# Kernel optimization log

Measured on AMD Instinct MI355X. Metric: run time of the kernel, lower is better.

The kernel has to match this reference:

```python
import jax, jax.numpy as jnp
import numpy as np

RES = 512
MAX_DEPTH = 100.0
AMBIENT = 0.3
LIGHT_STREN = 0.8
SHININESS = 16.0
EPS = 1e-8


def _unit(v):
    return v / (jnp.linalg.norm(v, axis=-1, keepdims=True) + EPS)


def setup_inputs() -> dict:
    key = jax.random.key(0)
    ks = jax.random.split(key, 8)
    B, N, M, TEX = 1, 512, 128, 512
    verts = jax.random.uniform(ks[0], (B, N, 3), minval=-1.0, maxval=1.0, dtype=jnp.float32)
    faces = jax.random.randint(ks[1], (B, M, 3), 0, N, dtype=jnp.int32)
    normals = jax.random.normal(ks[2], (B, M, 3, 3), dtype=jnp.float32)
    uvs = jax.random.uniform(ks[3], (B, M, 3, 2), dtype=jnp.float32)
    textures = jax.random.uniform(ks[4], (B, TEX, TEX, 3), dtype=jnp.float32)
    f = RES / 2.0
    K = jnp.array([[f, 0.0, RES / 2.0], [0.0, f, RES / 2.0], [0.0, 0.0, 1.0]], jnp.float32)
    Ks = jnp.broadcast_to(K, (B, 3, 3))
    RT = jnp.concatenate([jnp.eye(3, dtype=jnp.float32), jnp.array([[0.0], [0.0], [2.0]], jnp.float32)], axis=1)
    RTs = jnp.broadcast_to(RT, (B, 3, 4))
    view_dir = jax.random.normal(ks[5], (B, 3), dtype=jnp.float32)
    light_dir = jax.random.normal(ks[6], (B, 3), dtype=jnp.float32)
    return {"verts": verts, "faces": faces, "normals": normals, "uvs": uvs,
            "textures": textures, "Ks": Ks, "RTs": RTs, "view_dir": view_dir, "light_dir": light_dir}


def _render(verts, faces, normals, uvs, textures, Ks, RTs, view_dir, light_dir):
    B = verts.shape[0]
    # camera space: cam = R @ v + t
    cam = jnp.einsum('bij,bnj->bni', RTs[:, :, :3], verts) + RTs[:, None, :, 3]
    # orthographic projection to pixel coords
    x = Ks[:, None, 0, 0] * cam[..., 0] + Ks[:, None, 0, 2]
    y = Ks[:, None, 1, 1] * cam[..., 1] + Ks[:, None, 1, 2]
    xy = jnp.stack([x, y], -1)            # [B,N,2]
    z = cam[..., 2]                        # [B,N]
    gather_v = jax.vmap(lambda a, f: a[f])
    tv = gather_v(xy, faces)               # [B,M,3,2] screen-space triangle corners
    tz = gather_v(z, faces)                # [B,M,3]
    # pixel centers, row-major (p = row*RES + col)
    ii = jnp.arange(RES, dtype=jnp.float32) + 0.5
    py, px = jnp.meshgrid(ii, ii, indexing='ij')
    pix = jnp.stack([px.ravel(), py.ravel()], -1)   # [P,2]

    def edge(a, b, p):
        return (b[..., 0] - a[..., 0]) * (p[..., 1] - a[..., 1]) - (b[..., 1] - a[..., 1]) * (p[..., 0] - a[..., 0])

    v0, v1, v2 = tv[:, None, :, 0], tv[:, None, :, 1], tv[:, None, :, 2]  # [B,1,M,2]
    p = pix[None, :, None]                                               # [1,P,1,2]
    w0 = edge(v1, v2, p)                   # [B,P,M]
    w1 = edge(v2, v0, p)
    w2 = edge(v0, v1, p)
    area = w0 + w1 + w2
    inside = (((w0 >= 0) & (w1 >= 0) & (w2 >= 0)) | ((w0 <= 0) & (w1 <= 0) & (w2 <= 0))) & (jnp.abs(area) > EPS)
    inv_a = 1.0 / jnp.where(jnp.abs(area) > EPS, area, 1.0)
    zpix = (w0 * tz[:, None, :, 0] + w1 * tz[:, None, :, 1] + w2 * tz[:, None, :, 2]) * inv_a
    valid = inside & (zpix > 0)
    zc = jnp.where(valid, zpix, MAX_DEPTH)   # [B,P,M] candidate depths
    depth = jnp.min(zc, axis=-1)             # z-buffer result [B,P]
    win = jnp.argmin(zc, axis=-1)             # winning triangle per pixel [B,P]
    hit = depth < MAX_DEPTH

    # recompute barycentrics for the winning triangle only (avoids [B,P,M,3])
    gpick = jax.vmap(lambda a, i: a[i])
    tvw = gpick(tv, win)                      # [B,P,3,2]
    nw = gpick(normals, win)                  # [B,P,3,3]
    uvw = gpick(uvs, win)                     # [B,P,3,2]
    pp = pix[None]                            # [1,P,2]

    def e2(a, b):
        return (b[..., 0] - a[..., 0]) * (pp[..., 1] - a[..., 1]) - (b[..., 1] - a[..., 1]) * (pp[..., 0] - a[..., 0])

    u0 = e2(tvw[:, :, 1], tvw[:, :, 2])
    u1 = e2(tvw[:, :, 2], tvw[:, :, 0])
    u2 = e2(tvw[:, :, 0], tvw[:, :, 1])
    ar = u0 + u1 + u2
    inv2 = 1.0 / jnp.where(jnp.abs(ar) > EPS, ar, 1.0)
    bary = jnp.stack([u0, u1, u2], -1) * inv2[..., None]   # [B,P,3]
    nrm = _unit(jnp.einsum('bpk,bpkc->bpc', bary, nw))     # interpolated normal
    uv = jnp.einsum('bpk,bpkc->bpc', bary, uvw)            # interpolated uv [B,P,2]

    # bilinear texture sampling
    Ht, Wt = textures.shape[1], textures.shape[2]
    uu = jnp.clip(uv[..., 0], 0.0, 1.0) * (Wt - 1)
    vv = jnp.clip(uv[..., 1], 0.0, 1.0) * (Ht - 1)
    x0 = jnp.floor(uu).astype(jnp.int32)
    y0 = jnp.floor(vv).astype(jnp.int32)
    x1 = jnp.minimum(x0 + 1, Wt - 1)
    y1 = jnp.minimum(y0 + 1, Ht - 1)
    fx = (uu - x0.astype(jnp.float32))[..., None]
    fy = (vv - y0.astype(jnp.float32))[..., None]
    tget = jax.vmap(lambda t, a, b: t[a, b])
    col = (tget(textures, y0, x0) * (1 - fx) * (1 - fy) + tget(textures, y0, x1) * fx * (1 - fy)
           + tget(textures, y1, x0) * (1 - fx) * fy + tget(textures, y1, x1) * fx * fy)  # [B,P,3]

    # Lambert diffuse + Blinn-Phong specular
    ld = _unit(light_dir)
    vd = _unit(view_dir)
    diff = jnp.clip(jnp.einsum('bpc,bc->bp', nrm, ld), 0.0)
    h = _unit(ld + vd)
    spec = LIGHT_STREN * jnp.clip(jnp.einsum('bpc,bc->bp', nrm, h), 0.0) ** SHININESS
    shade = col * (AMBIENT + LIGHT_STREN * diff)[..., None] + spec[..., None]
    rgb = jnp.where(hit[..., None], shade, 0.0)

    depths = depth.reshape(B, RES, RES)
    rgbs = rgb.reshape(B, RES, RES, 3)
    masks = hit.reshape(B, RES, RES).astype(jnp.int32)
    return depths, rgbs, masks


def reference(verts, faces, normals, uvs, textures, Ks, RTs, view_dir, light_dir):
    return _render(verts, faces, normals, uvs, textures, Ks, RTs, view_dir, light_dir)
```

## Files before the change

kernel.cpp:

```cpp
#include <hip/hip_runtime.h>
#include <math.h>

#pragma clang fp contract(off)

#define RES         512
#define TILE        16
#define TILESX      (RES / TILE)
#define MAXF        128
#define MAX_DEPTH   100.0f
#define AMBIENT     0.3f
#define LIGHT_STREN 0.8f
#define EPSF        1e-8f
#define MARG        1.0f
#define ZGUARD      1e-3f

struct __attribute__((packed, aligned(4))) PF4 { float a, b, c, d; };
struct __attribute__((packed, aligned(4))) PF2 { float a, b; };
static __device__ __forceinline__ PF4 ld4(const float* p) { PF4 v; __builtin_memcpy(&v, p, 16); return v; }
static __device__ __forceinline__ PF2 ld2(const float* p) { PF2 v; __builtin_memcpy(&v, p, 8); return v; }

__global__ __launch_bounds__(256) void mesh_render_tiled(
    const float* __restrict__ verts,
    const int*   __restrict__ faces,
    const float* __restrict__ normals,
    const float* __restrict__ uvs,
    const float* __restrict__ tex,
    const float* __restrict__ Ks,
    const float* __restrict__ RTs,
    const float* __restrict__ view_dir,
    const float* __restrict__ light_dir,
    float* __restrict__ out,
    int M, int TEXW, int TEXH)
{
    __shared__ float4 smA[MAXF];
    __shared__ float4 smB[MAXF];
    __shared__ float2 smC[MAXF];
    __shared__ int    cid[MAXF];
    __shared__ int    scnt[2][8];
    __shared__ float  slit[6];

    const int tid = threadIdx.x;
    const int tx  = blockIdx.x % TILESX;
    const int ty  = blockIdx.x / TILESX;
    const float PX0 = (float)(tx * TILE) + 0.5f;
    const float PY0 = (float)(ty * TILE) + 0.5f;

    bool flag = false;
    int  bkt  = -1;
    float X0=0,Y0=0,Z0=0, X1=0,Y1=0,Z1=0, X2=0,Y2=0,Z2=0, MZ=0;
    unsigned long long bmask = 0;

    if (tid < MAXF) {
        if (tid < M) {
            const float r00 = RTs[0], r01 = RTs[1], r02 = RTs[2],  t0 = RTs[3];
            const float r10 = RTs[4], r11 = RTs[5], r12 = RTs[6],  t1 = RTs[7];
            const float r20 = RTs[8], r21 = RTs[9], r22 = RTs[10], t2 = RTs[11];
            const float k00 = Ks[0], k02 = Ks[2], k11 = Ks[4], k12 = Ks[5];
            float X[3], Y[3], Z[3];
            #pragma unroll
            for (int k = 0; k < 3; ++k) {
                int vi = faces[tid * 3 + k];
                float vx = verts[vi * 3 + 0];
                float vy = verts[vi * 3 + 1];
                float vz = verts[vi * 3 + 2];
                float cx = ((r00 * vx + r01 * vy) + r02 * vz) + t0;
                float cy = ((r10 * vx + r11 * vy) + r12 * vz) + t1;
                float cz = ((r20 * vx + r21 * vy) + r22 * vz) + t2;
                X[k] = k00 * cx + k02;
                Y[k] = k11 * cy + k12;
                Z[k] = cz;
            }
            X0=X[0]; Y0=Y[0]; Z0=Z[0]; X1=X[1]; Y1=Y[1]; Z1=Z[1];
            X2=X[2]; Y2=Y[2]; Z2=Z[2];
            MZ = fminf(fminf(Z0, Z1), Z2);

            float e0dx = X2-X1, e0dy = Y2-Y1;
            float e1dx = X0-X2, e1dy = Y0-Y2;
            float e2dx = X1-X0, e2dy = Y1-Y0;

            float minX = fminf(fminf(X0,X1),X2), maxX = fmaxf(fmaxf(X0,X1),X2);
            float minY = fminf(fminf(Y0,Y1),Y2), maxY = fmaxf(fmaxf(Y0,Y1),Y2);
            bool bb = (minX <= PX0 + 15.0f + MARG) && (maxX >= PX0 - MARG) &&
                      (minY <= PY0 + 15.0f + MARG) && (maxY >= PY0 - MARG);

            float wA0 = e0dx*(PY0-Y1) - e0dy*(PX0-X1);
            float wA1 = e1dx*(PY0-Y2) - e1dy*(PX0-X2);
            float wA2 = e2dx*(PY0-Y0) - e2dy*(PX0-X0);
            float area = (wA0 + wA1) + wA2;
            float amin = fminf(area, 0.0f) - MARG, amax = fmaxf(area, 0.0f) + MARG;

            float s0x = -e0dy*15.0f, s0y = e0dx*15.0f;
            float s1x = -e1dy*15.0f, s1y = e1dx*15.0f;
            float s2x = -e2dy*15.0f, s2y = e2dx*15.0f;
            float t0min = wA0 + fminf(s0x,0.f) + fminf(s0y,0.f);
            float t0max = wA0 + fmaxf(s0x,0.f) + fmaxf(s0y,0.f);
            float t1min = wA1 + fminf(s1x,0.f) + fminf(s1y,0.f);
            float t1max = wA1 + fmaxf(s1x,0.f) + fmaxf(s1y,0.f);
            float t2min = wA2 + fminf(s2x,0.f) + fminf(s2y,0.f);
            float t2max = wA2 + fmaxf(s2x,0.f) + fmaxf(s2y,0.f);
            bool ok0 = (t0max >= amin) && (t0min <= amax);
            bool ok1 = (t1max >= amin) && (t1min <= amax);
            bool ok2 = (t2max >= amin) && (t2min <= amax);
            flag = bb && ok0 && ok1 && ok2;
            if (flag) {
                int bq = (int)((MZ - 1.0f) * 4.0f);
                bkt = bq < 0 ? 0 : (bq > 7 ? 7 : bq);
            }
        }
        #pragma unroll
        for (int k = 0; k < 8; ++k) {
            unsigned long long mk = __ballot(flag && (bkt == k));
            if (bkt == k) bmask = mk;
            if ((tid & 63) == 0) scnt[tid >> 6][k] = __popcll(mk);
        }
    }
    if (tid == 128) {
        float lx = light_dir[0], ly = light_dir[1], lz = light_dir[2];
        float ll = sqrtf((lx*lx + ly*ly) + lz*lz) + 1e-8f;
        lx /= ll; ly /= ll; lz /= ll;
        float vx = view_dir[0], vy = view_dir[1], vz = view_dir[2];
        float vl = sqrtf((vx*vx + vy*vy) + vz*vz) + 1e-8f;
        vx /= vl; vy /= vl; vz /= vl;
        float hx = lx + vx, hy = ly + vy, hz = lz + vz;
        float hl = sqrtf((hx*hx + hy*hy) + hz*hz) + 1e-8f;
        slit[0] = lx; slit[1] = ly; slit[2] = lz;
        slit[3] = hx / hl; slit[4] = hy / hl; slit[5] = hz / hl;
    }
    __syncthreads();

    if (flag) {
        int wv = tid >> 6;
        int base = 0;
        for (int k = 0; k < bkt; ++k) base += scnt[0][k] + scnt[1][k];
        if (wv == 1) base += scnt[0][bkt];
        int pos = base + __popcll(bmask & ((1ull << (tid & 63)) - 1ull));
        smA[pos] = make_float4(X0, Y0, X1, Y1);
        smB[pos] = make_float4(X2, Y2, Z0, Z1);
        smC[pos] = make_float2(MZ - ZGUARD, Z2);
        cid[pos] = tid;
    }
    __syncthreads();

    int bend[8];
    {
        int acc = 0;
        #pragma unroll
        for (int k = 0; k < 8; ++k) { acc += scnt[0][k] + scnt[1][k]; bend[k] = acc; }
    }

    const int lx_ = tid & (TILE-1), ly_ = tid / TILE;
    const float px = PX0 + (float)lx_;
    const float py = PY0 + (float)ly_;
    const int p = (ty*TILE + ly_) * RES + (tx*TILE + lx_);

    float best = MAX_DEPTH;
    float w0s = 0.0f, w1s = 0.0f, w2s = 0.0f, invs = 1.0f;
    int winpos = -1;

    int i = 0;
    #pragma unroll 1
    for (int k = 0; k < 8; ++k) {
        const int e = bend[k];
        if (i >= e) continue;
        float lbk = (1.0f + 0.25f * (float)k) - ZGUARD;
        if (__all(lbk >= best)) break;
        for (; i < e; ++i) {
            const float2 c = smC[i];
            if (__all(c.x >= best)) continue;
            const float4 A = smA[i];
            const float4 B = smB[i];
            float w0 = (B.x - A.z) * (py - A.w) - (B.y - A.w) * (px - A.z);
            float w1 = (A.x - B.x) * (py - B.y) - (A.y - B.y) * (px - B.x);
            float w2 = (A.z - A.x) * (py - A.y) - (A.w - A.y) * (px - A.x);
            float area = (w0 + w1) + w2;
            float mn = fminf(fminf(w0, w1), w2);
            float mx = fmaxf(fmaxf(w0, w1), w2);
            bool nz = fabsf(area) > EPSF;
            bool inside = ((mn >= 0.0f) || (mx <= 0.0f)) && nz;
            float inva = __builtin_amdgcn_rcpf(nz ? area : 1.0f);
            float zpix = ((w0 * B.z + w1 * B.w) + w2 * c.y) * inva;
            float zc = (inside && (zpix > 0.0f)) ? zpix : MAX_DEPTH;
            if (zc < best) {
                best = zc; winpos = i;
                w0s = w0; w1s = w1; w2s = w2; invs = inva;
            }
        }
    }

    float r = 0.0f, g = 0.0f, b = 0.0f, mk = 0.0f, depth = MAX_DEPTH;
    if (winpos >= 0) {
        mk = 1.0f;
        depth = best;
        const int f = cid[winpos];
        float b0 = w0s * invs, b1 = w1s * invs, b2 = w2s * invs;

        const float* nw = normals + f * 9;
        PF4 n0 = ld4(nw); PF4 n1 = ld4(nw + 4); float n8 = nw[8];
        float nx  = (b0 * n0.a + b1 * n0.d) + b2 * n1.c;
        float ny  = (b0 * n0.b + b1 * n1.a) + b2 * n1.d;
        float nzv = (b0 * n0.c + b1 * n1.b) + b2 * n8;
        float nl  = __builtin_amdgcn_sqrtf((nx*nx + ny*ny) + nzv*nzv) + 1e-8f;
        float rn  = __builtin_amdgcn_rcpf(nl);
        nx *= rn; ny *= rn; nzv *= rn;

        const float* uvp = uvs + f * 6;
        PF4 u0 = ld4(uvp); PF2 u1 = ld2(uvp + 4);
        float uvx = (b0 * u0.a + b1 * u0.c) + b2 * u1.a;
        float uvy = (b0 * u0.b + b1 * u0.d) + b2 * u1.b;
        float uu = fminf(fmaxf(uvx, 0.0f), 1.0f) * (float)(TEXW - 1);
        float vv = fminf(fmaxf(uvy, 0.0f), 1.0f) * (float)(TEXH - 1);
        int x0 = (int)floorf(uu), y0 = (int)floorf(vv);
        int y1 = min(y0 + 1, TEXH - 1);
        float fx = uu - (float)x0, fy = vv - (float)y0;

        int xb = min(x0, TEXW - 2);
        bool xe = (x0 == TEXW - 1);
        const float* r0 = tex + (y0 * TEXW + xb) * 3;
        const float* r1 = tex + (y1 * TEXW + xb) * 3;
        PF4 a0 = ld4(r0); PF2 a1 = ld2(r0 + 4);
        PF4 c0 = ld4(r1); PF2 c1 = ld2(r1 + 4);
        float t00r = xe ? a0.d : a0.a, t00g = xe ? a1.a : a0.b, t00b = xe ? a1.b : a0.c;
        float t01r = a0.d,             t01g = a1.a,             t01b = a1.b;
        float t10r = xe ? c0.d : c0.a, t10g = xe ? c1.a : c0.b, t10b = xe ? c1.b : c0.c;
        float t11r = c0.d,             t11g = c1.a,             t11b = c1.b;

        float gx = 1.0f - fx, gy = 1.0f - fy;
        float cr = (((t00r*gx)*gy + (t01r*fx)*gy) + (t10r*gx)*fy) + (t11r*fx)*fy;
        float cg = (((t00g*gx)*gy + (t01g*fx)*gy) + (t10g*gx)*fy) + (t11g*fx)*fy;
        float cb = (((t00b*gx)*gy + (t01b*fx)*gy) + (t10b*gx)*fy) + (t11b*fx)*fy;

        float ldx = slit[0], ldy = slit[1], ldz = slit[2];
        float hx  = slit[3], hy  = slit[4], hz  = slit[5];
        float diff = fmaxf((nx*ldx + ny*ldy) + nzv*ldz, 0.0f);
        float sd   = fmaxf((nx*hx  + ny*hy)  + nzv*hz,  0.0f);
        float s2 = sd*sd, s4 = s2*s2, s8 = s4*s4, s16 = s8*s8;
        float spec  = LIGHT_STREN * s16;
        float scale = AMBIENT + LIGHT_STREN * diff;
        r = cr * scale + spec;
        g = cg * scale + spec;
        b = cb * scale + spec;
    }

    out[p] = depth;
    struct F3 { float x, y, z; };
    ((F3*)(out + RES * RES))[p] = F3{r, g, b};
    out[RES * RES * 4 + p] = mk;
}

extern "C" void kernel_launch(void* const* d_in, const int* in_sizes, int n_in,
                              void* d_out, int out_size, void* d_ws, size_t ws_size,
                              hipStream_t stream) {
    const float* verts     = (const float*)d_in[0];
    const int*   faces     = (const int*)  d_in[1];
    const float* normals   = (const float*)d_in[2];
    const float* uvs       = (const float*)d_in[3];
    const float* tex       = (const float*)d_in[4];
    const float* Ks        = (const float*)d_in[5];
    const float* RTs       = (const float*)d_in[6];
    const float* view_dir  = (const float*)d_in[7];
    const float* light_dir = (const float*)d_in[8];

    int M = in_sizes[1] / 3;
    if (M > MAXF) M = MAXF;
    const int texels = in_sizes[4] / 3;
    const int TEXW = (int)(sqrt((double)texels) + 0.5);
    const int TEXH = TEXW;

    const int blocks = TILESX * TILESX;
    mesh_render_tiled<<<blocks, 256, 0, stream>>>(
        verts, faces, normals, uvs, tex, Ks, RTs, view_dir, light_dir,
        (float*)d_out, M, TEXW, TEXH);
}
```

Baseline: 16.21 us.

## Split face list across two thread groups per pixel with 16x8 tiles

Tiles shrink to 16x8 pixels, so 256 threads now cover each pixel twice. Each half walks alternate faces, and the two partial depth/index results are merged through a packed 64-bit key in shared memory. Only the winning pixel's barycentrics are recomputed before shading, and the light and half-vector normalization moves from one shared-memory setup thread into each shading thread. This doubles the block count and halves the per-thread face loop, at the cost of extra syncs, a reduction step, and half the threads idling during shading.

Result: slower. 17.08 us (+5.4%).

```diff
diff --git a/kernel.cpp b/kernel.cpp
--- a/kernel.cpp
+++ b/kernel.cpp
@@ -4,8 +4,10 @@
 #pragma clang fp contract(off)
 
 #define RES         512
-#define TILE        16
-#define TILESX      (RES / TILE)
+#define TW          16
+#define THT         8
+#define TCOLS       (RES / TW)
+#define TROWS       (RES / THT)
 #define MAXF        128
 #define MAX_DEPTH   100.0f
 #define AMBIENT     0.3f
@@ -13,13 +15,15 @@
 #define EPSF        1e-8f
 #define MARG        1.0f
 #define ZGUARD      1e-3f
+#define EXTX        15.0f
+#define EXTY        7.0f
 
 struct __attribute__((packed, aligned(4))) PF4 { float a, b, c, d; };
 struct __attribute__((packed, aligned(4))) PF2 { float a, b; };
 static __device__ __forceinline__ PF4 ld4(const float* p) { PF4 v; __builtin_memcpy(&v, p, 16); return v; }
 static __device__ __forceinline__ PF2 ld2(const float* p) { PF2 v; __builtin_memcpy(&v, p, 8); return v; }
 
-__global__ __launch_bounds__(256) void mesh_render_tiled(
+__global__ __launch_bounds__(256, 8) void mesh_render_tiled(
     const float* __restrict__ verts,
     const int*   __restrict__ faces,
     const float* __restrict__ normals,
@@ -37,13 +41,13 @@
     __shared__ float2 smC[MAXF];
     __shared__ int    cid[MAXF];
     __shared__ int    scnt[2][8];
-    __shared__ float  slit[6];
+    __shared__ unsigned long long mkey[128];
 
     const int tid = threadIdx.x;
-    const int tx  = blockIdx.x % TILESX;
-    const int ty  = blockIdx.x / TILESX;
-    const float PX0 = (float)(tx * TILE) + 0.5f;
-    const float PY0 = (float)(ty * TILE) + 0.5f;
+    const int tX  = blockIdx.x & (TCOLS - 1);
+    const int tY  = blockIdx.x / TCOLS;
+    const float PX0 = (float)(tX * TW) + 0.5f;
+    const float PY0 = (float)(tY * THT) + 0.5f;
 
     bool flag = false;
     int  bkt  = -1;
@@ -80,8 +84,8 @@
 
             float minX = fminf(fminf(X0,X1),X2), maxX = fmaxf(fmaxf(X0,X1),X2);
             float minY = fminf(fminf(Y0,Y1),Y2), maxY = fmaxf(fmaxf(Y0,Y1),Y2);
-            bool bb = (minX <= PX0 + 15.0f + MARG) && (maxX >= PX0 - MARG) &&
-                      (minY <= PY0 + 15.0f + MARG) && (maxY >= PY0 - MARG);
+            bool bb = (minX <= PX0 + EXTX + MARG) && (maxX >= PX0 - MARG) &&
+                      (minY <= PY0 + EXTY + MARG) && (maxY >= PY0 - MARG);
 
             float wA0 = e0dx*(PY0-Y1) - e0dy*(PX0-X1);
             float wA1 = e1dx*(PY0-Y2) - e1dy*(PX0-X2);
@@ -89,18 +93,18 @@
             float area = (wA0 + wA1) + wA2;
             float amin = fminf(area, 0.0f) - MARG, amax = fmaxf(area, 0.0f) + MARG;
 
-            float s0x = -e0dy*15.0f, s0y = e0dx*15.0f;
-            float s1x = -e1dy*15.0f, s1y = e1dx*15.0f;
-            float s2x = -e2dy*15.0f, s2y = e2dx*15.0f;
-            float t0min = wA0 + fminf(s0x,0.f) + fminf(s0y,0.f);
-            float t0max = wA0 + fmaxf(s0x,0.f) + fmaxf(s0y,0.f);
-            float t1min = wA1 + fminf(s1x,0.f) + fminf(s1y,0.f);
-            float t1max = wA1 + fmaxf(s1x,0.f) + fmaxf(s1y,0.f);
-            float t2min = wA2 + fminf(s2x,0.f) + fminf(s2y,0.f);
-            float t2max = wA2 + fmaxf(s2x,0.f) + fmaxf(s2y,0.f);
-            bool ok0 = (t0max >= amin) && (t0min <= amax);
-            bool ok1 = (t1max >= amin) && (t1min <= amax);
-            bool ok2 = (t2max >= amin) && (t2min <= amax);
+            float s0x = -e0dy*EXTX, s0y = e0dx*EXTY;
+            float s1x = -e1dy*EXTX, s1y = e1dx*EXTY;
+            float s2x = -e2dy*EXTX, s2y = e2dx*EXTY;
+            float t0mn = wA0 + fminf(s0x,0.f) + fminf(s0y,0.f);
+            float t0mx = wA0 + fmaxf(s0x,0.f) + fmaxf(s0y,0.f);
+            float t1mn = wA1 + fminf(s1x,0.f) + fminf(s1y,0.f);
+            float t1mx = wA1 + fmaxf(s1x,0.f) + fmaxf(s1y,0.f);
+            float t2mn = wA2 + fminf(s2x,0.f) + fminf(s2y,0.f);
+            float t2mx = wA2 + fmaxf(s2x,0.f) + fmaxf(s2y,0.f);
+            bool ok0 = (t0mx >= amin) && (t0mn <= amax);
+            bool ok1 = (t1mx >= amin) && (t1mn <= amax);
+            bool ok2 = (t2mx >= amin) && (t2mn <= amax);
             flag = bb && ok0 && ok1 && ok2;
             if (flag) {
                 int bq = (int)((MZ - 1.0f) * 4.0f);
@@ -113,18 +117,6 @@
             if (bkt == k) bmask = mk;
             if ((tid & 63) == 0) scnt[tid >> 6][k] = __popcll(mk);
         }
-    }
-    if (tid == 128) {
-        float lx = light_dir[0], ly = light_dir[1], lz = light_dir[2];
-        float ll = sqrtf((lx*lx + ly*ly) + lz*lz) + 1e-8f;
-        lx /= ll; ly /= ll; lz /= ll;
-        float vx = view_dir[0], vy = view_dir[1], vz = view_dir[2];
-        float vl = sqrtf((vx*vx + vy*vy) + vz*vz) + 1e-8f;
-        vx /= vl; vy /= vl; vz /= vl;
-        float hx = lx + vx, hy = ly + vy, hz = lz + vz;
-        float hl = sqrtf((hx*hx + hy*hy) + hz*hz) + 1e-8f;
-        slit[0] = lx; slit[1] = ly; slit[2] = lz;
-        slit[3] = hx / hl; slit[4] = hy / hl; slit[5] = hz / hl;
     }
     __syncthreads();
 
@@ -148,23 +140,23 @@
         for (int k = 0; k < 8; ++k) { acc += scnt[0][k] + scnt[1][k]; bend[k] = acc; }
     }
 
-    const int lx_ = tid & (TILE-1), ly_ = tid / TILE;
+    const int pxid = tid & 127;
+    const int g    = tid >> 7;
+    const int lx_  = pxid & (TW - 1), ly_ = pxid >> 4;
     const float px = PX0 + (float)lx_;
     const float py = PY0 + (float)ly_;
-    const int p = (ty*TILE + ly_) * RES + (tx*TILE + lx_);
 
     float best = MAX_DEPTH;
-    float w0s = 0.0f, w1s = 0.0f, w2s = 0.0f, invs = 1.0f;
     int winpos = -1;
 
-    int i = 0;
+    int i = g;
     #pragma unroll 1
     for (int k = 0; k < 8; ++k) {
         const int e = bend[k];
         if (i >= e) continue;
         float lbk = (1.0f + 0.25f * (float)k) - ZGUARD;
         if (__all(lbk >= best)) break;
-        for (; i < e; ++i) {
+        for (; i < e; i += 2) {
             const float2 c = smC[i];
             if (__all(c.x >= best)) continue;
             const float4 A = smA[i];
@@ -180,71 +172,99 @@
             float inva = __builtin_amdgcn_rcpf(nz ? area : 1.0f);
             float zpix = ((w0 * B.z + w1 * B.w) + w2 * c.y) * inva;
             float zc = (inside && (zpix > 0.0f)) ? zpix : MAX_DEPTH;
-            if (zc < best) {
-                best = zc; winpos = i;
-                w0s = w0; w1s = w1; w2s = w2; invs = inva;
-            }
-        }
-    }
-
-    float r = 0.0f, g = 0.0f, b = 0.0f, mk = 0.0f, depth = MAX_DEPTH;
-    if (winpos >= 0) {
-        mk = 1.0f;
-        depth = best;
-        const int f = cid[winpos];
-        float b0 = w0s * invs, b1 = w1s * invs, b2 = w2s * invs;
-
-        const float* nw = normals + f * 9;
-        PF4 n0 = ld4(nw); PF4 n1 = ld4(nw + 4); float n8 = nw[8];
-        float nx  = (b0 * n0.a + b1 * n0.d) + b2 * n1.c;
-        float ny  = (b0 * n0.b + b1 * n1.a) + b2 * n1.d;
-        float nzv = (b0 * n0.c + b1 * n1.b) + b2 * n8;
-        float nl  = __builtin_amdgcn_sqrtf((nx*nx + ny*ny) + nzv*nzv) + 1e-8f;
-        float rn  = __builtin_amdgcn_rcpf(nl);
-        nx *= rn; ny *= rn; nzv *= rn;
-
-        const float* uvp = uvs + f * 6;
-        PF4 u0 = ld4(uvp); PF2 u1 = ld2(uvp + 4);
-        float uvx = (b0 * u0.a + b1 * u0.c) + b2 * u1.a;
-        float uvy = (b0 * u0.b + b1 * u0.d) + b2 * u1.b;
-        float uu = fminf(fmaxf(uvx, 0.0f), 1.0f) * (float)(TEXW - 1);
-        float vv = fminf(fmaxf(uvy, 0.0f), 1.0f) * (float)(TEXH - 1);
-        int x0 = (int)floorf(uu), y0 = (int)floorf(vv);
-        int y1 = min(y0 + 1, TEXH - 1);
-        float fx = uu - (float)x0, fy = vv - (float)y0;
-
-        int xb = min(x0, TEXW - 2);
-        bool xe = (x0 == TEXW - 1);
-        const float* r0 = tex + (y0 * TEXW + xb) * 3;
-        const float* r1 = tex + (y1 * TEXW + xb) * 3;
-        PF4 a0 = ld4(r0); PF2 a1 = ld2(r0 + 4);
-        PF4 c0 = ld4(r1); PF2 c1 = ld2(r1 + 4);
-        float t00r = xe ? a0.d : a0.a, t00g = xe ? a1.a : a0.b, t00b = xe ? a1.b : a0.c;
-        float t01r = a0.d,             t01g = a1.a,             t01b = a1.b;
-        float t10r = xe ? c0.d : c0.a, t10g = xe ? c1.a : c0.b, t10b = xe ? c1.b : c0.c;
-        float t11r = c0.d,             t11g = c1.a,             t11b = c1.b;
-
-        float gx = 1.0f - fx, gy = 1.0f - fy;
-        float cr = (((t00r*gx)*gy + (t01r*fx)*gy) + (t10r*gx)*fy) + (t11r*fx)*fy;
-        float cg = (((t00g*gx)*gy + (t01g*fx)*gy) + (t10g*gx)*fy) + (t11g*fx)*fy;
-        float cb = (((t00b*gx)*gy + (t01b*fx)*gy) + (t10b*gx)*fy) + (t11b*fx)*fy;
-
-        float ldx = slit[0], ldy = slit[1], ldz = slit[2];
-        float hx  = slit[3], hy  = slit[4], hz  = slit[5];
-        float diff = fmaxf((nx*ldx + ny*ldy) + nzv*ldz, 0.0f);
-        float sd   = fmaxf((nx*hx  + ny*hy)  + nzv*hz,  0.0f);
-        float s2 = sd*sd, s4 = s2*s2, s8 = s4*s4, s16 = s8*s8;
-        float spec  = LIGHT_STREN * s16;
-        float scale = AMBIENT + LIGHT_STREN * diff;
-        r = cr * scale + spec;
-        g = cg * scale + spec;
-        b = cb * scale + spec;
-    }
-
-    out[p] = depth;
-    struct F3 { float x, y, z; };
-    ((F3*)(out + RES * RES))[p] = F3{r, g, b};
-    out[RES * RES * 4 + p] = mk;
+            if (zc < best) { best = zc; winpos = i; }
+        }
+    }
+
+    unsigned long long key =
+        ((unsigned long long)__float_as_uint(best) << 32) |
+        (unsigned long long)(winpos >= 0 ? (unsigned)winpos : 0xFFFFFFFFu);
+    if (g == 0) mkey[pxid] = key;
+    __syncthreads();
+    if (g == 1 && key < mkey[pxid]) mkey[pxid] = key;
+    __syncthreads();
+
+    if (tid < 128) {
+        const unsigned long long kk = mkey[tid];
+        const unsigned pos = (unsigned)(kk & 0xFFFFFFFFu);
+        const float depth = __uint_as_float((unsigned)(kk >> 32));
+        const int p = (tY*THT + ly_) * RES + tX*TW + lx_;
+
+        float r = 0.0f, gg = 0.0f, b = 0.0f, mk = 0.0f;
+        if (pos != 0xFFFFFFFFu) {
+            mk = 1.0f;
+            const float4 A = smA[pos];
+            const float4 B = smB[pos];
+            const float2 c = smC[pos];
+            const int f = cid[pos];
+            float w0 = (B.x - A.z) * (py - A.w) - (B.y - A.w) * (px - A.z);
+            float w1 = (A.x - B.x) * (py - B.y) - (A.y - B.y) * (px - B.x);
+            float w2 = (A.z - A.x) * (py - A.y) - (A.w - A.y) * (px - A.x);
+            float area = (w0 + w1) + w2;
+            bool nz = fabsf(area) > EPSF;
+            float inva = __builtin_amdgcn_rcpf(nz ? area : 1.0f);
+            float b0 = w0 * inva, b1 = w1 * inva, b2 = w2 * inva;
+
+            const float* nw = normals + f * 9;
+            PF4 n0 = ld4(nw); PF4 n1 = ld4(nw + 4); float n8 = nw[8];
+            float nx  = (b0 * n0.a + b1 * n0.d) + b2 * n1.c;
+            float ny  = (b0 * n0.b + b1 * n1.a) + b2 * n1.d;
+            float nzv = (b0 * n0.c + b1 * n1.b) + b2 * n8;
+            float nl  = __builtin_amdgcn_sqrtf((nx*nx + ny*ny) + nzv*nzv) + 1e-8f;
+            float rn  = __builtin_amdgcn_rcpf(nl);
+            nx *= rn; ny *= rn; nzv *= rn;
+
+            const float* uvp = uvs + f * 6;
+            PF4 u0 = ld4(uvp); PF2 u1 = ld2(uvp + 4);
+            float uvx = (b0 * u0.a + b1 * u0.c) + b2 * u1.a;
+            float uvy = (b0 * u0.b + b1 * u0.d) + b2 * u1.b;
+            float uu = fminf(fmaxf(uvx, 0.0f), 1.0f) * (float)(TEXW - 1);
+            float vv = fminf(fmaxf(uvy, 0.0f), 1.0f) * (float)(TEXH - 1);
+            int x0 = (int)floorf(uu), y0 = (int)floorf(vv);
+            int y1 = min(y0 + 1, TEXH - 1);
+            float fx = uu - (float)x0, fy = vv - (float)y0;
+
+            int xb = min(x0, TEXW - 2);
+            bool xe = (x0 == TEXW - 1);
+            const float* r0 = tex + (y0 * TEXW + xb) * 3;
+            const float* r1 = tex + (y1 * TEXW + xb) * 3;
+            PF4 a0 = ld4(r0); PF2 a1 = ld2(r0 + 4);
+            PF4 c0 = ld4(r1); PF2 c1 = ld2(r1 + 4);
+            float t00r = xe ? a0.d : a0.a, t00g = xe ? a1.a : a0.b, t00b = xe ? a1.b : a0.c;
+            float t01r = a0.d,             t01g = a1.a,             t01b = a1.b;
+            float t10r = xe ? c0.d : c0.a, t10g = xe ? c1.a : c0.b, t10b = xe ? c1.b : c0.c;
+            float t11r = c0.d,             t11g = c1.a,             t11b = c1.b;
+
+            float gx = 1.0f - fx, gy = 1.0f - fy;
+            float cr = (((t00r*gx)*gy + (t01r*fx)*gy) + (t10r*gx)*fy) + (t11r*fx)*fy;
+            float cg = (((t00g*gx)*gy + (t01g*fx)*gy) + (t10g*gx)*fy) + (t11g*fx)*fy;
+            float cb = (((t00b*gx)*gy + (t01b*fx)*gy) + (t10b*gx)*fy) + (t11b*fx)*fy;
+
+            float ldx = light_dir[0], ldy = light_dir[1], ldz = light_dir[2];
+            float ll = sqrtf((ldx*ldx + ldy*ldy) + ldz*ldz) + 1e-8f;
+            ldx /= ll; ldy /= ll; ldz /= ll;
+            float vdx = view_dir[0], vdy = view_dir[1], vdz = view_dir[2];
+            float vl = sqrtf((vdx*vdx + vdy*vdy) + vdz*vdz) + 1e-8f;
+            vdx /= vl; vdy /= vl; vdz /= vl;
+            float hx = ldx + vdx, hy = ldy + vdy, hz = ldz + vdz;
+            float hl = sqrtf((hx*hx + hy*hy) + hz*hz) + 1e-8f;
+            hx /= hl; hy /= hl; hz /= hl;
+
+            float diff = fmaxf((nx*ldx + ny*ldy) + nzv*ldz, 0.0f);
+            float sd   = fmaxf((nx*hx  + ny*hy)  + nzv*hz,  0.0f);
+            float s2 = sd*sd, s4 = s2*s2, s8 = s4*s4, s16 = s8*s8;
+            float spec  = LIGHT_STREN * s16;
+            float scale = AMBIENT + LIGHT_STREN * diff;
+            r  = cr * scale + spec;
+            gg = cg * scale + spec;
+            b  = cb * scale + spec;
+        }
+
+        out[p] = depth;
+        struct F3 { float x, y, z; };
+        ((F3*)(out + RES * RES))[p] = F3{r, gg, b};
+        out[RES * RES * 4 + p] = mk;
+    }
 }
 
 extern "C" void kernel_launch(void* const* d_in, const int* in_sizes, int n_in,
@@ -266,7 +286,7 @@
     const int TEXW = (int)(sqrt((double)texels) + 0.5);
     const int TEXH = TEXW;
 
-    const int blocks = TILESX * TILESX;
+    const int blocks = TCOLS * TROWS;
     mesh_render_tiled<<<blocks, 256, 0, stream>>>(
         verts, faces, normals, uvs, tex, Ks, RTs, view_dir, light_dir,
         (float*)d_out, M, TEXW, TEXH);
```
